# Kernel optimization log

Hardware: AMD Instinct MI355X
Metric: run time of the kernel (lower is better)

Reference implementation:

```python
import jax, jax.numpy as jnp
import numpy as np

N = 100_000
E = 1_600_000
IN_DIM = 21
HID = 256
OUT = 256


def setup_inputs() -> dict:
    key = jax.random.key(0)
    ks = jax.random.split(key, 10)
    node_scalar = jax.random.normal(ks[0], (N, IN_DIM), dtype=jnp.float32)
    edge_index = jax.random.randint(ks[1], (2, E), 0, N, dtype=jnp.int64)
    s_in = 1.0 / np.sqrt(IN_DIM)
    s_h = 1.0 / np.sqrt(HID)
    W_in = jax.random.uniform(ks[2], (IN_DIM, HID), jnp.float32, -s_in, s_in)
    b_in = jax.random.uniform(ks[3], (HID,), jnp.float32, -s_in, s_in)
    W_self = jax.random.uniform(ks[4], (HID, HID), jnp.float32, -s_h, s_h)
    b_self = jax.random.uniform(ks[5], (HID,), jnp.float32, -s_h, s_h)
    W_nei = jax.random.uniform(ks[6], (HID, HID), jnp.float32, -s_h, s_h)
    b_nei = jax.random.uniform(ks[7], (HID,), jnp.float32, -s_h, s_h)
    W_out = jax.random.uniform(ks[8], (HID, OUT), jnp.float32, -s_h, s_h)
    b_out = jax.random.uniform(ks[9], (OUT,), jnp.float32, -s_h, s_h)
    return {
        "node_scalar": node_scalar,
        "W_in": W_in, "b_in": b_in,
        "W_self": W_self, "b_self": b_self,
        "W_nei": W_nei, "b_nei": b_nei,
        "W_out": W_out, "b_out": b_out,
        "edge_index": edge_index,
    }


def reference(node_scalar, W_in, b_in, W_self, b_self, W_nei, b_nei, W_out, b_out, edge_index):
    # x = relu(Linear(node_scalar)); dropout is identity in eval mode
    x = jax.nn.relu(node_scalar @ W_in + b_in)           # (N, H)
    n = x.shape[0]
    src, dst = edge_index[0], edge_index[1]
    msg = x[src]                                          # (E, H) gather
    agg = jax.ops.segment_sum(msg, dst, num_segments=n)   # (N, H) scatter-add
    deg = jax.ops.segment_sum(jnp.ones((dst.shape[0],), dtype=x.dtype), dst, num_segments=n)
    agg = agg / jnp.maximum(deg, 1.0)[:, None]            # degree mean (clamp_min 1)
    h = jax.nn.relu(x @ W_self + b_self + agg @ W_nei + b_nei)
    g = h.mean(axis=0)                                    # global mean pool -> (H,)
    return g @ W_out + b_out                              # (OUT,)
```

## Files before the change

### kernel.cpp

```cpp
#include <hip/hip_runtime.h>
#include <hip/hip_bf16.h>

#define HID 256
#define IND 21
#define ASTR 40
#define PB 3200
#define MAXB 512

typedef short short8 __attribute__((ext_vector_type(8)));
typedef float floatx4 __attribute__((ext_vector_type(4)));
typedef float floatx2 __attribute__((ext_vector_type(2)));

__device__ inline unsigned short f2bf(float f) {
  __hip_bfloat16 h = __float2bfloat16(f);
  union { __hip_bfloat16 h; unsigned short u; } c;
  c.h = h;
  return c.u;
}

__device__ inline unsigned int pk_bf16_trunc(floatx2 p) {
  union { float f; unsigned int u; } a, b;
  a.f = p.x; b.f = p.y;
  return (b.u & 0xffff0000u) | (a.u >> 16);
}

__device__ inline void acc8p(uint2 v, floatx2* a) {
  a[0] += __builtin_amdgcn_cvt_pk_f32_fp8((int)v.x, false);
  a[1] += __builtin_amdgcn_cvt_pk_f32_fp8((int)v.x, true);
  a[2] += __builtin_amdgcn_cvt_pk_f32_fp8((int)v.y, false);
  a[3] += __builtin_amdgcn_cvt_pk_f32_fp8((int)v.y, true);
}

__global__ __launch_bounds__(256) void k_front(
    const float* __restrict__ ns, const float* __restrict__ Win,
    const float* __restrict__ bin, unsigned int* __restrict__ xq,
    const float* __restrict__ Wself, const float* __restrict__ Wnei,
    unsigned short* __restrict__ WcT,
    const int* __restrict__ dst, int* __restrict__ bcnt,
    int N, int E, int nb2, int G1) {
  int blk = blockIdx.x;
  int tid = threadIdx.x;
  if (blk < G1) {
    __shared__ float s[8][IND];
    __shared__ float fx[8][257];
    int nb = blk * 8;
    if (tid < 8 * IND) {
      int idx = nb * IND + tid;
      s[tid / IND][tid % IND] = (idx < N * IND) ? ns[idx] : 0.f;
    }
    float w[IND];
#pragma unroll
    for (int k = 0; k < IND; k++) w[k] = Win[k * HID + tid];
    float b = bin[tid];
    __syncthreads();
#pragma unroll
    for (int j = 0; j < 8; j++) {
      float acc = b;
#pragma unroll
      for (int k = 0; k < IND; k++) acc += s[j][k] * w[k];
      fx[j][tid] = acc > 0.f ? acc : 0.f;
    }
    __syncthreads();
#pragma unroll
    for (int t = 0; t < 2; t++) {
      int wi = tid + t * 256;
      int j = wi >> 6, cw = wi & 63;
      int node = nb + j;
      if (node < N) {
        const float* fp = &fx[j][cw * 4];
        int lo = __builtin_amdgcn_cvt_pk_fp8_f32(fp[0], fp[1], 0, false);
        int full = __builtin_amdgcn_cvt_pk_fp8_f32(fp[2], fp[3], lo, true);
        xq[(size_t)node * 64 + cw] = (unsigned int)full;
      }
    }
  } else if (blk < G1 + 256) {
    int n = blk - G1;
#pragma unroll
    for (int t = 0; t < 2; t++) {
      int k = tid + t * 256;
      float v = (k < HID) ? Wself[k * HID + n] : Wnei[(k - HID) * HID + n];
      WcT[n * 512 + k] = f2bf(v);
    }
  } else {
    __shared__ int lh[MAXB];
    int e0 = (blk - G1 - 256) * PB;
    for (int b = tid; b < nb2; b += 256) lh[b] = 0;
    __syncthreads();
    int c = min(PB, E - e0);
    for (int i = tid; i < c; i += 256) atomicAdd(&lh[dst[e0 + i] >> 8], 1);
    __syncthreads();
    for (int b = tid; b < nb2; b += 256)
      if (lh[b]) atomicAdd(&bcnt[b], lh[b]);
  }
}

__global__ __launch_bounds__(512) void k_bscan(
    const int* __restrict__ bcnt, int* __restrict__ bbase, int* __restrict__ bcur,
    int* __restrict__ row_start, int E, int N, int nb2) {
  __shared__ int ts[512];
  int tid = threadIdx.x;
  int v = (tid < nb2) ? bcnt[tid] : 0;
  ts[tid] = v;
  __syncthreads();
  for (int off = 1; off < 512; off <<= 1) {
    int t = (tid >= off) ? ts[tid - off] : 0;
    __syncthreads();
    ts[tid] += t;
    __syncthreads();
  }
  if (tid < nb2) { bbase[tid] = ts[tid] - v; bcur[tid] = ts[tid] - v; }
  if (tid == 0) { bbase[nb2] = E; row_start[N] = E; }
}

__global__ __launch_bounds__(256) void k_part(
    const int* __restrict__ src, const int* __restrict__ dst,
    int* __restrict__ bcur, uint2* __restrict__ ebuf, int E, int nb2) {
  __shared__ int lh[MAXB];
  int tid = threadIdx.x;
  int e0 = blockIdx.x * PB;
  for (int b = tid; b < nb2; b += 256) lh[b] = 0;
  __syncthreads();
  int cnt = min(PB, E - e0);
  for (int i = tid; i < cnt; i += 256) atomicAdd(&lh[dst[e0 + i] >> 8], 1);
  __syncthreads();
  for (int b = tid; b < nb2; b += 256) {
    int c = lh[b];
    lh[b] = (c > 0) ? atomicAdd(&bcur[b], c) : 0;
  }
  __syncthreads();
  for (int i = tid; i < cnt; i += 256) {
    int s = src[e0 + i];
    int d = dst[e0 + i];
    int pos = atomicAdd(&lh[d >> 8], 1);
    ebuf[pos] = make_uint2((unsigned)s, (unsigned)d);
  }
}

__global__ __launch_bounds__(256) void k_fill2(
    const uint2* __restrict__ ebuf, const int* __restrict__ bbase,
    int* __restrict__ row_start, int* __restrict__ csr, int N) {
  __shared__ int lcnt[256];
  __shared__ int lcur[256];
  __shared__ int ts[256];
  int b = blockIdx.x;
  int tid = threadIdx.x;
  int start = bbase[b], end = bbase[b + 1];
  lcnt[tid] = 0;
  __syncthreads();
  for (int i = start + tid; i < end; i += 256)
    atomicAdd(&lcnt[ebuf[i].y & 255], 1);
  __syncthreads();
  int v = lcnt[tid];
  ts[tid] = v;
  __syncthreads();
  for (int off = 1; off < 256; off <<= 1) {
    int t = (tid >= off) ? ts[tid - off] : 0;
    __syncthreads();
    ts[tid] += t;
    __syncthreads();
  }
  int excl = start + ts[tid] - v;
  int node = (b << 8) + tid;
  if (node < N) row_start[node] = excl;
  lcur[tid] = excl;
  __syncthreads();
  for (int i = start + tid; i < end; i += 256) {
    uint2 e = ebuf[i];
    int pos = atomicAdd(&lcur[e.y & 255], 1);
    csr[pos] = (int)e.x;
  }
}

__global__ __launch_bounds__(256) void k_agg(
    const uint2* __restrict__ xq, const int* __restrict__ csr,
    const int* __restrict__ row_start, uint2* __restrict__ aggq, int N) {
  int wid = (int)((blockIdx.x * (unsigned)blockDim.x + threadIdx.x) >> 6);
  int lane = threadIdx.x & 63;
  int half = lane >> 5;
  int l32 = lane & 31;
  if (wid >= N) return;
  int start = row_start[wid];
  int end = row_start[wid + 1];
  int c = end - start;
  floatx2 a[4], b[4], d[4], e[4];
#pragma unroll
  for (int j = 0; j < 4; j++) {
    a[j] = (floatx2){0.f, 0.f}; b[j] = (floatx2){0.f, 0.f};
    d[j] = (floatx2){0.f, 0.f}; e[j] = (floatx2){0.f, 0.f};
  }

  int i = 0;
  for (; i + 8 <= c; i += 8) {
    int s0 = csr[start + i + half];
    int s1 = csr[start + i + 2 + half];
    int s2 = csr[start + i + 4 + half];
    int s3 = csr[start + i + 6 + half];
    uint2 v0 = xq[(size_t)s0 * 32 + l32];
    uint2 v1 = xq[(size_t)s1 * 32 + l32];
    uint2 v2 = xq[(size_t)s2 * 32 + l32];
    uint2 v3 = xq[(size_t)s3 * 32 + l32];
    acc8p(v0, a); acc8p(v1, b); acc8p(v2, d); acc8p(v3, e);
  }
  for (; i + 2 <= c; i += 2) {
    int s0 = csr[start + i + half];
    uint2 v0 = xq[(size_t)s0 * 32 + l32];
    acc8p(v0, a);
  }
  if ((c & 1) && half == 0) {
    int s0 = csr[start + c - 1];
    uint2 v0 = xq[(size_t)s0 * 32 + l32];
    acc8p(v0, a);
  }
#pragma unroll
  for (int j = 0; j < 4; j++) a[j] += b[j] + d[j] + e[j];

  float f[8];
#pragma unroll
  for (int j = 0; j < 4; j++) { f[2 * j] = a[j].x; f[2 * j + 1] = a[j].y; }
#pragma unroll
  for (int j = 0; j < 8; j++) f[j] += __shfl_xor(f[j], 32);

  if (half == 0) {
    float inv = 1.0f / fmaxf((float)c, 1.0f);
#pragma unroll
    for (int j = 0; j < 8; j++) f[j] *= inv;
    int lo0 = __builtin_amdgcn_cvt_pk_fp8_f32(f[0], f[1], 0, false);
    int w0  = __builtin_amdgcn_cvt_pk_fp8_f32(f[2], f[3], lo0, true);
    int lo1 = __builtin_amdgcn_cvt_pk_fp8_f32(f[4], f[5], 0, false);
    int w1  = __builtin_amdgcn_cvt_pk_fp8_f32(f[6], f[7], lo1, true);
    aggq[(size_t)wid * 32 + l32] = make_uint2((unsigned)w0, (unsigned)w1);
  }
}

__global__ __launch_bounds__(256, 2) void k_h(
    const unsigned char* __restrict__ xq8, const unsigned char* __restrict__ aggq8,
    const unsigned short* __restrict__ WcT, const float* __restrict__ bself,
    const float* __restrict__ bnei, float* __restrict__ gsum, int N) {
  __shared__ __align__(16) unsigned short As[128 * ASTR];
  __shared__ __align__(16) unsigned short Bs[256 * ASTR];
  __shared__ float colsum[256];
  int tid = threadIdx.x;
  int rowBase = blockIdx.x * 128;
  int lane = tid & 63;
  int wid = tid >> 6;
  int wr = wid >> 1, wc = wid & 1;
  int n16 = lane & 15, quad = lane >> 4;

  colsum[tid] = 0.f;

  floatx4 acc[4][8];
#pragma unroll
  for (int i = 0; i < 4; i++)
#pragma unroll
    for (int j = 0; j < 8; j++) acc[i][j] = (floatx4){0.f, 0.f, 0.f, 0.f};

  int ar = tid >> 1;
  int as = tid & 1;
  int gr = rowBase + ar;
  if (gr >= N) gr = N - 1;

  for (int k0 = 0; k0 < 512; k0 += 32) {
    const unsigned char* abase = (k0 < HID) ? xq8 : aggq8;
    int kc = k0 & 255;
    uint4 v = *(const uint4*)(abase + (size_t)gr * HID + kc + as * 16);
    unsigned int w[8];
    {
      unsigned int src4[4] = {v.x, v.y, v.z, v.w};
#pragma unroll
      for (int j = 0; j < 4; j++) {
        floatx2 p0 = __builtin_amdgcn_cvt_pk_f32_fp8((int)src4[j], false);
        floatx2 p1 = __builtin_amdgcn_cvt_pk_f32_fp8((int)src4[j], true);
        w[2 * j] = pk_bf16_trunc(p0);
        w[2 * j + 1] = pk_bf16_trunc(p1);
      }
    }
    *(uint4*)(&As[ar * ASTR + as * 16]) = make_uint4(w[0], w[1], w[2], w[3]);
    *(uint4*)(&As[ar * ASTR + as * 16 + 8]) = make_uint4(w[4], w[5], w[6], w[7]);
#pragma unroll
    for (int j = 0; j < 4; j++) {
      int idx = tid + j * 256;
      int r = idx >> 2;
      int s = idx & 3;
      uint4 vb = *(const uint4*)(WcT + (size_t)r * 512 + k0 + s * 8);
      *(uint4*)(&Bs[r * ASTR + s * 8]) = vb;
    }
    __syncthreads();

    short8 af[4];
#pragma unroll
    for (int rt = 0; rt < 4; rt++)
      af[rt] = *(const short8*)&As[(wr * 64 + rt * 16 + n16) * ASTR + quad * 8];
#pragma unroll
    for (int ct = 0; ct < 8; ct++) {
      short8 bf = *(const short8*)&Bs[(wc * 128 + ct * 16 + n16) * ASTR + quad * 8];
#pragma unroll
      for (int rt = 0; rt < 4; rt++)
        acc[rt][ct] = __builtin_amdgcn_mfma_f32_16x16x32_bf16(
            af[rt], bf, acc[rt][ct], 0, 0, 0);
    }
    __syncthreads();
  }

#pragma unroll
  for (int ct = 0; ct < 8; ct++) {
    int gcol = wc * 128 + ct * 16 + n16;
    float bb = bself[gcol] + bnei[gcol];
    float psum = 0.f;
#pragma unroll
    for (int rt = 0; rt < 4; rt++) {
#pragma unroll
      for (int r = 0; r < 4; r++) {
        int row = rowBase + wr * 64 + rt * 16 + quad * 4 + r;
        float v = acc[rt][ct][r] + bb;
        v = v > 0.f ? v : 0.f;
        if (row < N) psum += v;
      }
    }
    atomicAdd(&colsum[gcol], psum);
  }
  __syncthreads();
  atomicAdd(&gsum[tid], colsum[tid]);
}

__global__ __launch_bounds__(HID) void k_out(
    const float* __restrict__ gsum, const float* __restrict__ Wout,
    const float* __restrict__ bout, float* __restrict__ out, float invN) {
  __shared__ float g[HID];
  int c = threadIdx.x;
  g[c] = gsum[c] * invN;
  __syncthreads();
  float acc = bout[c];
#pragma unroll 8
  for (int k = 0; k < HID; k++) acc += g[k] * Wout[k * HID + c];
  out[c] = acc;
}

extern "C" void kernel_launch(void* const* d_in, const int* in_sizes, int n_in,
                              void* d_out, int out_size, void* d_ws, size_t ws_size,
                              hipStream_t stream) {
  const float* ns    = (const float*)d_in[0];
  const float* Win   = (const float*)d_in[1];
  const float* bin   = (const float*)d_in[2];
  const float* Wself = (const float*)d_in[3];
  const float* bself = (const float*)d_in[4];
  const float* Wnei  = (const float*)d_in[5];
  const float* bnei  = (const float*)d_in[6];
  const float* Wout  = (const float*)d_in[7];
  const float* bout  = (const float*)d_in[8];
  const int*   eidx  = (const int*)d_in[9];

  int N = in_sizes[0] / IND;
  int E = in_sizes[9] / 2;
  const int* src = eidx;
  const int* dst = eidx + E;
  int nb2 = (N + 255) >> 8;

  unsigned int* xq    = (unsigned int*)d_ws;
  unsigned int* aggq  = xq + (size_t)N * 64;
  unsigned short* WcT = (unsigned short*)(aggq + (size_t)N * 64);
  int* csr       = (int*)(WcT + 256 * 512);
  uint2* ebuf    = (uint2*)(csr + E);
  int* row_start = (int*)(ebuf + E);
  int* bcnt      = row_start + N + 1;
  int* bbase     = bcnt + MAXB;
  int* bcur      = bbase + MAXB + 1;
  float* gsum    = (float*)(bcur + MAXB);

  hipMemsetAsync(bcnt, 0, MAXB * sizeof(int), stream);
  hipMemsetAsync(gsum, 0, HID * sizeof(float), stream);

  int G1 = (N + 7) / 8;
  int pgrid = (E + PB - 1) / PB;
  k_front<<<G1 + 256 + pgrid, 256, 0, stream>>>(
      ns, Win, bin, xq, Wself, Wnei, WcT, dst, bcnt, N, E, nb2, G1);

  k_bscan<<<1, 512, 0, stream>>>(bcnt, bbase, bcur, row_start, E, N, nb2);
  k_part<<<pgrid, 256, 0, stream>>>(src, dst, bcur, ebuf, E, nb2);
  k_fill2<<<nb2, 256, 0, stream>>>(ebuf, bbase, row_start, csr, N);

  int agrid = (N + 3) / 4;
  k_agg<<<agrid, 256, 0, stream>>>((const uint2*)xq, csr, row_start,
                                   (uint2*)aggq, N);

  int hgrid = (N + 127) / 128;
  k_h<<<hgrid, 256, 0, stream>>>((const unsigned char*)xq,
                                 (const unsigned char*)aggq,
                                 WcT, bself, bnei, gsum, N);

  k_out<<<1, HID, 0, stream>>>(gsum, Wout, bout, (float*)d_out, 1.0f / (float)N);
}
```

Measured before the change: 322.0 us.

## Prefetch next K-tile in k_h, widen K step, pack edge buffer to 32 bits

The k_h GEMM now steps K in 64-wide chunks (stride 72) and loads the next chunk's A and B tiles into registers while the current chunk's MFMAs run, so global latency overlaps compute and the number of barriers is halved. The edge partition buffer packs src<<8 | dst&255 into one 32-bit word instead of a uint2, halving the ebuf traffic in k_part and k_fill2. The partition block size PB is doubled. In exchange, register and LDS pressure rise in k_h (eight extra uint4 prefetch registers, larger shared tiles), which may cut occupancy. The packing assumes source indices fit in 24 bits.

```diff
diff --git a/kernel.cpp b/kernel.cpp
--- a/kernel.cpp
+++ b/kernel.cpp
@@ -3,8 +3,8 @@
 
 #define HID 256
 #define IND 21
-#define ASTR 40
-#define PB 3200
+#define ASTR2 72
+#define PB 6400
 #define MAXB 512
 
 typedef short short8 __attribute__((ext_vector_type(8)));
@@ -29,6 +29,15 @@
   a[1] += __builtin_amdgcn_cvt_pk_f32_fp8((int)v.x, true);
   a[2] += __builtin_amdgcn_cvt_pk_f32_fp8((int)v.y, false);
   a[3] += __builtin_amdgcn_cvt_pk_f32_fp8((int)v.y, true);
+}
+
+__device__ inline void dec16(uint4 v, unsigned int* w) {
+  unsigned int s4[4] = {v.x, v.y, v.z, v.w};
+#pragma unroll
+  for (int j = 0; j < 4; j++) {
+    w[2 * j] = pk_bf16_trunc(__builtin_amdgcn_cvt_pk_f32_fp8((int)s4[j], false));
+    w[2 * j + 1] = pk_bf16_trunc(__builtin_amdgcn_cvt_pk_f32_fp8((int)s4[j], true));
+  }
 }
 
 __global__ __launch_bounds__(256) void k_front(
@@ -114,7 +123,7 @@
 
 __global__ __launch_bounds__(256) void k_part(
     const int* __restrict__ src, const int* __restrict__ dst,
-    int* __restrict__ bcur, uint2* __restrict__ ebuf, int E, int nb2) {
+    int* __restrict__ bcur, unsigned int* __restrict__ ebuf, int E, int nb2) {
   __shared__ int lh[MAXB];
   int tid = threadIdx.x;
   int e0 = blockIdx.x * PB;
@@ -132,12 +141,12 @@
     int s = src[e0 + i];
     int d = dst[e0 + i];
     int pos = atomicAdd(&lh[d >> 8], 1);
-    ebuf[pos] = make_uint2((unsigned)s, (unsigned)d);
+    ebuf[pos] = ((unsigned)s << 8) | ((unsigned)d & 255u);
   }
 }
 
 __global__ __launch_bounds__(256) void k_fill2(
-    const uint2* __restrict__ ebuf, const int* __restrict__ bbase,
+    const unsigned int* __restrict__ ebuf, const int* __restrict__ bbase,
     int* __restrict__ row_start, int* __restrict__ csr, int N) {
   __shared__ int lcnt[256];
   __shared__ int lcur[256];
@@ -148,7 +157,7 @@
   lcnt[tid] = 0;
   __syncthreads();
   for (int i = start + tid; i < end; i += 256)
-    atomicAdd(&lcnt[ebuf[i].y & 255], 1);
+    atomicAdd(&lcnt[ebuf[i] & 255u], 1);
   __syncthreads();
   int v = lcnt[tid];
   ts[tid] = v;
@@ -165,9 +174,9 @@
   lcur[tid] = excl;
   __syncthreads();
   for (int i = start + tid; i < end; i += 256) {
-    uint2 e = ebuf[i];
-    int pos = atomicAdd(&lcur[e.y & 255], 1);
-    csr[pos] = (int)e.x;
+    unsigned int e = ebuf[i];
+    int pos = atomicAdd(&lcur[e & 255u], 1);
+    csr[pos] = (int)(e >> 8);
   }
 }
 
@@ -188,7 +197,6 @@
     a[j] = (floatx2){0.f, 0.f}; b[j] = (floatx2){0.f, 0.f};
     d[j] = (floatx2){0.f, 0.f}; e[j] = (floatx2){0.f, 0.f};
   }
-
   int i = 0;
   for (; i + 8 <= c; i += 8) {
     int s0 = csr[start + i + half];
@@ -236,8 +244,8 @@
     const unsigned char* __restrict__ xq8, const unsigned char* __restrict__ aggq8,
     const unsigned short* __restrict__ WcT, const float* __restrict__ bself,
     const float* __restrict__ bnei, float* __restrict__ gsum, int N) {
-  __shared__ __align__(16) unsigned short As[128 * ASTR];
-  __shared__ __align__(16) unsigned short Bs[256 * ASTR];
+  __shared__ __align__(16) unsigned short As[128 * ASTR2];
+  __shared__ __align__(16) unsigned short Bs[256 * ASTR2];
   __shared__ float colsum[256];
   int tid = threadIdx.x;
   int rowBase = blockIdx.x * 128;
@@ -255,48 +263,66 @@
     for (int j = 0; j < 8; j++) acc[i][j] = (floatx4){0.f, 0.f, 0.f, 0.f};
 
   int ar = tid >> 1;
-  int as = tid & 1;
+  int ah = tid & 1;
   int gr = rowBase + ar;
   if (gr >= N) gr = N - 1;
-
-  for (int k0 = 0; k0 < 512; k0 += 32) {
-    const unsigned char* abase = (k0 < HID) ? xq8 : aggq8;
-    int kc = k0 & 255;
-    uint4 v = *(const uint4*)(abase + (size_t)gr * HID + kc + as * 16);
-    unsigned int w[8];
+  size_t abyte = (size_t)gr * HID + ah * 32;
+
+  uint4 pa0, pa1, pb[8];
+  {
+    const unsigned char* ab = xq8;
+    pa0 = *(const uint4*)(ab + abyte);
+    pa1 = *(const uint4*)(ab + abyte + 16);
+#pragma unroll
+    for (int j = 0; j < 8; j++) {
+      int idx = tid + j * 256;
+      pb[j] = *(const uint4*)(WcT + (size_t)(idx >> 3) * 512 + (idx & 7) * 8);
+    }
+  }
+
+  for (int it = 0; it < 8; it++) {
+    int k0 = it * 64;
     {
-      unsigned int src4[4] = {v.x, v.y, v.z, v.w};
-#pragma unroll
-      for (int j = 0; j < 4; j++) {
-        floatx2 p0 = __builtin_amdgcn_cvt_pk_f32_fp8((int)src4[j], false);
-        floatx2 p1 = __builtin_amdgcn_cvt_pk_f32_fp8((int)src4[j], true);
-        w[2 * j] = pk_bf16_trunc(p0);
-        w[2 * j + 1] = pk_bf16_trunc(p1);
+      unsigned int w[8];
+      dec16(pa0, w);
+      *(uint4*)(&As[ar * ASTR2 + ah * 32]) = make_uint4(w[0], w[1], w[2], w[3]);
+      *(uint4*)(&As[ar * ASTR2 + ah * 32 + 8]) = make_uint4(w[4], w[5], w[6], w[7]);
+      dec16(pa1, w);
+      *(uint4*)(&As[ar * ASTR2 + ah * 32 + 16]) = make_uint4(w[0], w[1], w[2], w[3]);
+      *(uint4*)(&As[ar * ASTR2 + ah * 32 + 24]) = make_uint4(w[4], w[5], w[6], w[7]);
+#pragma unroll
+      for (int j = 0; j < 8; j++) {
+        int idx = tid + j * 256;
+        *(uint4*)(&Bs[(idx >> 3) * ASTR2 + (idx & 7) * 8]) = pb[j];
       }
     }
-    *(uint4*)(&As[ar * ASTR + as * 16]) = make_uint4(w[0], w[1], w[2], w[3]);
-    *(uint4*)(&As[ar * ASTR + as * 16 + 8]) = make_uint4(w[4], w[5], w[6], w[7]);
-#pragma unroll
-    for (int j = 0; j < 4; j++) {
-      int idx = tid + j * 256;
-      int r = idx >> 2;
-      int s = idx & 3;
-      uint4 vb = *(const uint4*)(WcT + (size_t)r * 512 + k0 + s * 8);
-      *(uint4*)(&Bs[r * ASTR + s * 8]) = vb;
-    }
-    __syncthreads();
-
-    short8 af[4];
-#pragma unroll
-    for (int rt = 0; rt < 4; rt++)
-      af[rt] = *(const short8*)&As[(wr * 64 + rt * 16 + n16) * ASTR + quad * 8];
-#pragma unroll
-    for (int ct = 0; ct < 8; ct++) {
-      short8 bf = *(const short8*)&Bs[(wc * 128 + ct * 16 + n16) * ASTR + quad * 8];
+    __syncthreads();
+    if (it < 7) {
+      int kn = k0 + 64;
+      const unsigned char* ab = (kn < HID) ? xq8 : aggq8;
+      size_t off = abyte + (kn & 255);
+      pa0 = *(const uint4*)(ab + off);
+      pa1 = *(const uint4*)(ab + off + 16);
+#pragma unroll
+      for (int j = 0; j < 8; j++) {
+        int idx = tid + j * 256;
+        pb[j] = *(const uint4*)(WcT + (size_t)(idx >> 3) * 512 + kn + (idx & 7) * 8);
+      }
+    }
+#pragma unroll
+    for (int kk = 0; kk < 64; kk += 32) {
+      short8 af[4];
 #pragma unroll
       for (int rt = 0; rt < 4; rt++)
-        acc[rt][ct] = __builtin_amdgcn_mfma_f32_16x16x32_bf16(
-            af[rt], bf, acc[rt][ct], 0, 0, 0);
+        af[rt] = *(const short8*)&As[(wr * 64 + rt * 16 + n16) * ASTR2 + kk + quad * 8];
+#pragma unroll
+      for (int ct = 0; ct < 8; ct++) {
+        short8 bf = *(const short8*)&Bs[(wc * 128 + ct * 16 + n16) * ASTR2 + kk + quad * 8];
+#pragma unroll
+        for (int rt = 0; rt < 4; rt++)
+          acc[rt][ct] = __builtin_amdgcn_mfma_f32_16x16x32_bf16(
+              af[rt], bf, acc[rt][ct], 0, 0, 0);
+      }
     }
     __syncthreads();
   }
@@ -359,7 +385,7 @@
   unsigned int* aggq  = xq + (size_t)N * 64;
   unsigned short* WcT = (unsigned short*)(aggq + (size_t)N * 64);
   int* csr       = (int*)(WcT + 256 * 512);
-  uint2* ebuf    = (uint2*)(csr + E);
+  unsigned int* ebuf = (unsigned int*)(csr + E);
   int* row_start = (int*)(ebuf + E);
   int* bcnt      = row_start + N + 1;
   int* bbase     = bcnt + MAXB;
```

Result: slower. 344.0 us (+6.8%).
